# Optimization experiments

Hardware: AMD Instinct MI355X
Metric: run time of the kernel (lower is better)

Reference implementation:

```python
import jax, jax.numpy as jnp
import numpy as np

B, C, H, W = 4, 64, 64, 64
CQ = C // 8

def setup_inputs() -> dict:
    key = jax.random.key(0)
    ks = jax.random.split(key, 8)
    s = 1.0 / np.sqrt(C)
    return {
        "x": jax.random.normal(ks[0], (B, C, H, W), dtype=jnp.float32),
        "Wq": jax.random.normal(ks[1], (CQ, C), dtype=jnp.float32) * s,
        "bq": jax.random.normal(ks[2], (CQ,), dtype=jnp.float32) * 0.01,
        "Wk": jax.random.normal(ks[3], (CQ, C), dtype=jnp.float32) * s,
        "bk": jax.random.normal(ks[4], (CQ,), dtype=jnp.float32) * 0.01,
        "Wv": jax.random.normal(ks[5], (C, C), dtype=jnp.float32) * s,
        "bv": jax.random.normal(ks[6], (C,), dtype=jnp.float32) * 0.01,
        "gamma": jax.random.normal(ks[7], (1,), dtype=jnp.float32) * 0.1,
    }

def reference(x, Wq, bq, Wk, bk, Wv, bv, gamma):
    b, c, h, w = x.shape
    n = h * w
    xf = x.reshape(b, c, n)  # [B, C, N]
    # 1x1 convs are pointwise channel projections
    q = jnp.einsum('oc,bcn->bon', Wq, xf) + bq[None, :, None]  # [B, CQ, N]
    k = jnp.einsum('oc,bcn->bon', Wk, xf) + bk[None, :, None]  # [B, CQ, N]
    v = jnp.einsum('oc,bcn->bon', Wv, xf) + bv[None, :, None]  # [B, C, N]
    energy = jnp.einsum('bcn,bcm->bnm', q, k)                  # [B, N, N]
    attn = jax.nn.softmax(energy, axis=-1)
    out = jnp.einsum('bcm,bnm->bcn', v, attn)                  # [B, C, N]
    out = out.reshape(b, c, h, w)
    return gamma[0] * out + x
```

## Files before the change

### kernel.cpp

```cpp
#include <hip/hip_runtime.h>
#include <hip/hip_bf16.h>


typedef __attribute__((ext_vector_type(8))) short short8;
typedef __attribute__((ext_vector_type(4))) float f32x4;
typedef unsigned short ushort_t;

#define NSEQ 4096
#define LOG2E 1.4426950408889634f

__device__ __forceinline__ unsigned pk_bf16(float lo, float hi) {
  union { __hip_bfloat16 b; unsigned short u; } cl, ch;
  cl.b = __float2bfloat16(lo);
  ch.b = __float2bfloat16(hi);
  return (unsigned)cl.u | ((unsigned)ch.u << 16);
}

__global__ __launch_bounds__(256, 4) void proj_kernel(
    const float* __restrict__ x,
    const float* __restrict__ Wq, const float* __restrict__ bq,
    const float* __restrict__ Wk, const float* __restrict__ bk,
    const float* __restrict__ Wv, const float* __restrict__ bv,
    ushort_t* __restrict__ Qb, ushort_t* __restrict__ Kb,
    ushort_t* __restrict__ Vb)
{
  const int tid  = threadIdx.x;
  const int lane = tid & 63;
  const int w    = __builtin_amdgcn_readfirstlane(tid >> 6);
  const int blk  = blockIdx.x;
  const int quarter = blk & 3;
  const int g    = (blk >> 2) & 63;
  const int b    = blk >> 8;
  const int n    = g * 64 + lane;

  const float* xb = x + (size_t)(b * 64) * NSEQ + n;
  const int co0 = quarter * 16 + w * 4;
  const float* w0 = Wv + (co0 + 0) * 64;
  const float* w1 = Wv + (co0 + 1) * 64;
  const float* w2 = Wv + (co0 + 2) * 64;
  const float* w3 = Wv + (co0 + 3) * 64;
  const int p = quarter * 4 + w;
  const float* wr = (p < 8) ? (Wq + p * 64) : (Wk + (p - 8) * 64);
  float a0 = bv[co0 + 0], a1 = bv[co0 + 1], a2 = bv[co0 + 2], a3 = bv[co0 + 3];
  float aq = (p < 8) ? bq[p] : bk[p - 8];

#pragma unroll
  for (int kc = 0; kc < 64; kc += 8) {
    float xv[8];
#pragma unroll
    for (int i = 0; i < 8; ++i) xv[i] = xb[(size_t)(kc + i) * NSEQ];
#pragma unroll
    for (int i = 0; i < 8; ++i) {
      const float xk = xv[i];
      a0 += w0[kc + i] * xk;
      a1 += w1[kc + i] * xk;
      a2 += w2[kc + i] * xk;
      a3 += w3[kc + i] * xk;
      aq += wr[kc + i] * xk;
    }
  }

  union { __hip_bfloat16 h; ushort_t u; } cv;
  ushort_t* vt = Vb + ((size_t)(b * 128 + (n >> 5)) * 64 + co0) * 32 + (n & 31);
  cv.h = __float2bfloat16(a0); vt[0]  = cv.u;
  cv.h = __float2bfloat16(a1); vt[32] = cv.u;
  cv.h = __float2bfloat16(a2); vt[64] = cv.u;
  cv.h = __float2bfloat16(a3); vt[96] = cv.u;

  ushort_t* qk = ((p < 8) ? Qb : Kb) + ((size_t)(b * NSEQ + n)) * 8 + (p & 7);
  cv.h = __float2bfloat16(aq); *qk = cv.u;
}

__global__ __launch_bounds__(512, 4) void attn_kernel(
    const ushort_t* __restrict__ Qb, const ushort_t* __restrict__ Kb,
    const ushort_t* __restrict__ Vb, const float* __restrict__ x,
    const float* __restrict__ gamma, float* __restrict__ out)
{
  __shared__ unsigned P_lds[2][8][2][256];
  __shared__ float buf[4][64][36];

  const int tid  = threadIdx.x;
  const int wave = __builtin_amdgcn_readfirstlane(tid >> 6);
  const int lane = tid & 63;
  const int q16  = lane & 15;
  const int quad = lane >> 4;
  const int blk  = blockIdx.x;
  const int b    = blk >> 7;
  const int n0   = (blk & 127) << 5;
  const int mbase = wave << 9;

  const short8 z8 = {0, 0, 0, 0, 0, 0, 0, 0};
  short8 qfA = *(const short8*)(Qb + ((size_t)(b * NSEQ + n0 + q16)) * 8);
  short8 qfB = *(const short8*)(Qb + ((size_t)(b * NSEQ + n0 + 16 + q16)) * 8);
  if (quad != 0) { qfA = z8; qfB = z8; }

  const char* kbase = (const char*)(Kb + ((size_t)(b * NSEQ + mbase + q16)) * 8);
  const char* vbase = (const char*)(Vb + ((size_t)(b * 128 + (mbase >> 5)) * 64) * 32);
  const int voff = q16 * 64 + quad * 16;

  const int sw    = (q16 ^ (q16 >> 2)) & 3;
  const int row16 = q16 * 16;
  const int d0 = 2 * quad, d2 = 8 + 2 * quad;
  const int w00 = row16 + (((d0 >> 2) ^ sw) << 2) + (d0 & 3);
  const int w01 = row16 + ((((d0 + 1) >> 2) ^ sw) << 2) + ((d0 + 1) & 3);
  const int w10 = row16 + (((d2 >> 2) ^ sw) << 2) + (d2 & 3);
  const int w11 = row16 + ((((d2 + 1) >> 2) ^ sw) << 2) + ((d2 + 1) & 3);
  const int rdo = row16 + ((quad ^ sw) << 2);

  f32x4 aA0 = {0.f, 0.f, 0.f, 0.f};
  f32x4 aA1 = aA0, aA2 = aA0, aA3 = aA0;
  f32x4 aB0 = aA0, aB1 = aA0, aB2 = aA0, aB3 = aA0;
  float lA = 0.f, lB = 0.f;

  short8 kf0 = *(const short8*)(kbase);
  short8 kf1 = *(const short8*)(kbase + 256);
  short8 vf0 = *(const short8*)(vbase + voff);
  short8 vf1 = *(const short8*)(vbase + voff + 1024);
  short8 vf2 = *(const short8*)(vbase + voff + 2048);
  short8 vf3 = *(const short8*)(vbase + voff + 3072);

#pragma unroll 2
  for (int t = 0; t < 16; ++t) {
    const int tn = (t + 1 < 16) ? (t + 1) : 15;
    const size_t ko = (size_t)tn * 512;
    const size_t vo = (size_t)tn * 4096 + voff;
    short8 nk0 = *(const short8*)(kbase + ko);
    short8 nk1 = *(const short8*)(kbase + ko + 256);
    short8 nv0 = *(const short8*)(vbase + vo);
    short8 nv1 = *(const short8*)(vbase + vo + 1024);
    short8 nv2 = *(const short8*)(vbase + vo + 2048);
    short8 nv3 = *(const short8*)(vbase + vo + 3072);

    const f32x4 z = {0.f, 0.f, 0.f, 0.f};
    f32x4 s0 = __builtin_amdgcn_mfma_f32_16x16x32_bf16(kf0, qfA, z, 0, 0, 0);
    f32x4 s1 = __builtin_amdgcn_mfma_f32_16x16x32_bf16(kf1, qfA, z, 0, 0, 0);
    f32x4 s2 = __builtin_amdgcn_mfma_f32_16x16x32_bf16(kf0, qfB, z, 0, 0, 0);
    f32x4 s3 = __builtin_amdgcn_mfma_f32_16x16x32_bf16(kf1, qfB, z, 0, 0, 0);

    float pA0 = __builtin_amdgcn_exp2f(s0[0] * LOG2E);
    float pA1 = __builtin_amdgcn_exp2f(s0[1] * LOG2E);
    float pA2 = __builtin_amdgcn_exp2f(s0[2] * LOG2E);
    float pA3 = __builtin_amdgcn_exp2f(s0[3] * LOG2E);
    float pA4 = __builtin_amdgcn_exp2f(s1[0] * LOG2E);
    float pA5 = __builtin_amdgcn_exp2f(s1[1] * LOG2E);
    float pA6 = __builtin_amdgcn_exp2f(s1[2] * LOG2E);
    float pA7 = __builtin_amdgcn_exp2f(s1[3] * LOG2E);
    float pB0 = __builtin_amdgcn_exp2f(s2[0] * LOG2E);
    float pB1 = __builtin_amdgcn_exp2f(s2[1] * LOG2E);
    float pB2 = __builtin_amdgcn_exp2f(s2[2] * LOG2E);
    float pB3 = __builtin_amdgcn_exp2f(s2[3] * LOG2E);
    float pB4 = __builtin_amdgcn_exp2f(s3[0] * LOG2E);
    float pB5 = __builtin_amdgcn_exp2f(s3[1] * LOG2E);
    float pB6 = __builtin_amdgcn_exp2f(s3[2] * LOG2E);
    float pB7 = __builtin_amdgcn_exp2f(s3[3] * LOG2E);
    lA += ((pA0 + pA1) + (pA2 + pA3)) + ((pA4 + pA5) + (pA6 + pA7));
    lB += ((pB0 + pB1) + (pB2 + pB3)) + ((pB4 + pB5) + (pB6 + pB7));

    unsigned* pbA = &P_lds[t & 1][wave][0][0];
    unsigned* pbB = &P_lds[t & 1][wave][1][0];
    pbA[w00] = pk_bf16(pA0, pA1);
    pbA[w01] = pk_bf16(pA2, pA3);
    pbA[w10] = pk_bf16(pA4, pA5);
    pbA[w11] = pk_bf16(pA6, pA7);
    pbB[w00] = pk_bf16(pB0, pB1);
    pbB[w01] = pk_bf16(pB2, pB3);
    pbB[w10] = pk_bf16(pB4, pB5);
    pbB[w11] = pk_bf16(pB6, pB7);
    const short8 pfA = *(const short8*)(pbA + rdo);
    const short8 pfB = *(const short8*)(pbB + rdo);

    aA0 = __builtin_amdgcn_mfma_f32_16x16x32_bf16(pfA, vf0, aA0, 0, 0, 0);
    aA1 = __builtin_amdgcn_mfma_f32_16x16x32_bf16(pfA, vf1, aA1, 0, 0, 0);
    aA2 = __builtin_amdgcn_mfma_f32_16x16x32_bf16(pfA, vf2, aA2, 0, 0, 0);
    aA3 = __builtin_amdgcn_mfma_f32_16x16x32_bf16(pfA, vf3, aA3, 0, 0, 0);
    aB0 = __builtin_amdgcn_mfma_f32_16x16x32_bf16(pfB, vf0, aB0, 0, 0, 0);
    aB1 = __builtin_amdgcn_mfma_f32_16x16x32_bf16(pfB, vf1, aB1, 0, 0, 0);
    aB2 = __builtin_amdgcn_mfma_f32_16x16x32_bf16(pfB, vf2, aB2, 0, 0, 0);
    aB3 = __builtin_amdgcn_mfma_f32_16x16x32_bf16(pfB, vf3, aB3, 0, 0, 0);

    kf0 = nk0; kf1 = nk1;
    vf0 = nv0; vf1 = nv1; vf2 = nv2; vf3 = nv3;
  }

  lA += __shfl_xor(lA, 16); lA += __shfl_xor(lA, 32);
  lB += __shfl_xor(lB, 16); lB += __shfl_xor(lB, 32);

  f32x4 aAs[4] = {aA0, aA1, aA2, aA3};
  f32x4 aBs[4] = {aB0, aB1, aB2, aB3};

  if (wave >= 4) {
    float* d = &buf[wave - 4][lane][0];
#pragma unroll
    for (int j = 0; j < 4; ++j)
#pragma unroll
      for (int r = 0; r < 4; ++r) {
        d[j * 4 + r]      = aAs[j][r];
        d[16 + j * 4 + r] = aBs[j][r];
      }
    d[32] = lA; d[33] = lB;
  }
  __syncthreads();
  if (wave < 4) {
    float* d = &buf[wave][lane][0];
#pragma unroll
    for (int j = 0; j < 4; ++j)
#pragma unroll
      for (int r = 0; r < 4; ++r) {
        aAs[j][r] += d[j * 4 + r];
        aBs[j][r] += d[16 + j * 4 + r];
      }
    lA += d[32]; lB += d[33];
#pragma unroll
    for (int j = 0; j < 4; ++j)
#pragma unroll
      for (int r = 0; r < 4; ++r) {
        d[j * 4 + r]      = aAs[j][r];
        d[16 + j * 4 + r] = aBs[j][r];
      }
    d[32] = lA; d[33] = lB;
  }
  __syncthreads();

  const int qt = wave >> 2;
  const int cg = wave & 3;
  float fr[4] = {0.f, 0.f, 0.f, 0.f};
  float lt = 0.f;
#pragma unroll
  for (int w2 = 0; w2 < 4; ++w2) {
    lt += buf[w2][lane][32 + qt];
#pragma unroll
    for (int r = 0; r < 4; ++r) fr[r] += buf[w2][lane][qt * 16 + cg * 4 + r];
  }

  const float g = gamma[0];
  const int c = cg * 16 + q16;
#pragma unroll
  for (int r = 0; r < 4; ++r) {
    const int rr = quad * 4 + r;
    const float lr = __shfl(lt, rr);
    const size_t idx = ((size_t)(b * 64 + c)) * NSEQ + n0 + qt * 16 + rr;
    out[idx] = g * (fr[r] / lr) + x[idx];
  }
}

extern "C" void kernel_launch(void* const* d_in, const int* in_sizes, int n_in,
                              void* d_out, int out_size, void* d_ws, size_t ws_size,
                              hipStream_t stream) {
  (void)in_sizes; (void)n_in; (void)out_size; (void)ws_size;
  const float* x     = (const float*)d_in[0];
  const float* Wq    = (const float*)d_in[1];
  const float* bq    = (const float*)d_in[2];
  const float* Wk    = (const float*)d_in[3];
  const float* bk    = (const float*)d_in[4];
  const float* Wv    = (const float*)d_in[5];
  const float* bv    = (const float*)d_in[6];
  const float* gamma = (const float*)d_in[7];
  float* out = (float*)d_out;

  ushort_t* Qb = (ushort_t*)d_ws;
  ushort_t* Kb = (ushort_t*)((char*)d_ws + (256u << 10));
  ushort_t* Vb = (ushort_t*)((char*)d_ws + (512u << 10));

  hipLaunchKernelGGL(proj_kernel, dim3(1024), dim3(256), 0, stream,
                     x, Wq, bq, Wk, bk, Wv, bv, Qb, Kb, Vb);
  hipLaunchKernelGGL(attn_kernel, dim3(512), dim3(512), 0, stream,
                     Qb, Kb, Vb, x, gamma, out);
}
```

Before: 97.23 us.

## Keep softmax probabilities in registers via permuted K rows and transposed PV MFMA

The attention kernel now permutes the K row order and swaps the operands of the PV MFMA, so the exponentiated scores can be packed straight into MFMA operand registers. This drops the LDS round trip (and its swizzle) that previously re-laid out P each tile. The log2(e) factor is folded into Q inside the projection kernel, so the per-element multiply before exp2 goes away. The projection kernel is also restructured so each wave computes 16 V channels plus 4 Q/K channels per pixel, with packed 8-byte Q/K stores and a quarter of the blocks. The epilogue indexing changes to match the transposed accumulator layout. Risk: the fewer, larger projection blocks give less parallelism and more registers per thread.

```diff
diff --git a/kernel.cpp b/kernel.cpp
--- a/kernel.cpp
+++ b/kernel.cpp
@@ -16,7 +16,7 @@
   return (unsigned)cl.u | ((unsigned)ch.u << 16);
 }
 
-__global__ __launch_bounds__(256, 4) void proj_kernel(
+__global__ __launch_bounds__(256) void proj_kernel(
     const float* __restrict__ x,
     const float* __restrict__ Wq, const float* __restrict__ bq,
     const float* __restrict__ Wk, const float* __restrict__ bk,
@@ -28,21 +28,23 @@
   const int lane = tid & 63;
   const int w    = __builtin_amdgcn_readfirstlane(tid >> 6);
   const int blk  = blockIdx.x;
-  const int quarter = blk & 3;
-  const int g    = (blk >> 2) & 63;
-  const int b    = blk >> 8;
-  const int n    = g * 64 + lane;
+  const int b    = blk >> 6;
+  const int n    = (blk & 63) * 64 + lane;
 
   const float* xb = x + (size_t)(b * 64) * NSEQ + n;
-  const int co0 = quarter * 16 + w * 4;
-  const float* w0 = Wv + (co0 + 0) * 64;
-  const float* w1 = Wv + (co0 + 1) * 64;
-  const float* w2 = Wv + (co0 + 2) * 64;
-  const float* w3 = Wv + (co0 + 3) * 64;
-  const int p = quarter * 4 + w;
-  const float* wr = (p < 8) ? (Wq + p * 64) : (Wk + (p - 8) * 64);
-  float a0 = bv[co0 + 0], a1 = bv[co0 + 1], a2 = bv[co0 + 2], a3 = bv[co0 + 3];
-  float aq = (p < 8) ? bq[p] : bk[p - 8];
+
+  const int cv0 = w * 16;
+  float av[16];
+#pragma unroll
+  for (int j = 0; j < 16; ++j) av[j] = bv[cv0 + j];
+
+  const bool isq = (w < 2);
+  const int qkb  = (w & 1) * 4;
+  const float* Wr = isq ? Wq : Wk;
+  const float* br = isq ? bq : bk;
+  float aqk[4];
+#pragma unroll
+  for (int j = 0; j < 4; ++j) aqk[j] = br[qkb + j];
 
 #pragma unroll
   for (int kc = 0; kc < 64; kc += 8) {
@@ -52,23 +54,30 @@
 #pragma unroll
     for (int i = 0; i < 8; ++i) {
       const float xk = xv[i];
-      a0 += w0[kc + i] * xk;
-      a1 += w1[kc + i] * xk;
-      a2 += w2[kc + i] * xk;
-      a3 += w3[kc + i] * xk;
-      aq += wr[kc + i] * xk;
+#pragma unroll
+      for (int j = 0; j < 16; ++j) av[j] += Wv[(cv0 + j) * 64 + kc + i] * xk;
+#pragma unroll
+      for (int j = 0; j < 4; ++j) aqk[j] += Wr[(qkb + j) * 64 + kc + i] * xk;
     }
   }
 
   union { __hip_bfloat16 h; ushort_t u; } cv;
-  ushort_t* vt = Vb + ((size_t)(b * 128 + (n >> 5)) * 64 + co0) * 32 + (n & 31);
-  cv.h = __float2bfloat16(a0); vt[0]  = cv.u;
-  cv.h = __float2bfloat16(a1); vt[32] = cv.u;
-  cv.h = __float2bfloat16(a2); vt[64] = cv.u;
-  cv.h = __float2bfloat16(a3); vt[96] = cv.u;
-
-  ushort_t* qk = ((p < 8) ? Qb : Kb) + ((size_t)(b * NSEQ + n)) * 8 + (p & 7);
-  cv.h = __float2bfloat16(aq); *qk = cv.u;
+  ushort_t* vt = Vb + ((size_t)(b * 128 + (n >> 5)) * 64 + cv0) * 32 + (n & 31);
+#pragma unroll
+  for (int j = 0; j < 16; ++j) {
+    cv.h = __float2bfloat16(av[j]);
+    vt[j * 32] = cv.u;
+  }
+
+  if (isq) {
+#pragma unroll
+    for (int j = 0; j < 4; ++j) aqk[j] *= LOG2E;
+  }
+  union { unsigned u[2]; ulong1 l; } pkd;
+  pkd.u[0] = pk_bf16(aqk[0], aqk[1]);
+  pkd.u[1] = pk_bf16(aqk[2], aqk[3]);
+  ushort_t* qk = (isq ? Qb : Kb) + ((size_t)(b * NSEQ + n)) * 8 + qkb;
+  *(ulong1*)qk = pkd.l;
 }
 
 __global__ __launch_bounds__(512, 4) void attn_kernel(
@@ -76,7 +85,6 @@
     const ushort_t* __restrict__ Vb, const float* __restrict__ x,
     const float* __restrict__ gamma, float* __restrict__ out)
 {
-  __shared__ unsigned P_lds[2][8][2][256];
   __shared__ float buf[4][64][36];
 
   const int tid  = threadIdx.x;
@@ -94,18 +102,10 @@
   short8 qfB = *(const short8*)(Qb + ((size_t)(b * NSEQ + n0 + 16 + q16)) * 8);
   if (quad != 0) { qfA = z8; qfB = z8; }
 
-  const char* kbase = (const char*)(Kb + ((size_t)(b * NSEQ + mbase + q16)) * 8);
+  const int mperm = 8 * (q16 >> 2) + (q16 & 3);
+  const char* kbase = (const char*)(Kb + ((size_t)(b * NSEQ + mbase + mperm)) * 8);
   const char* vbase = (const char*)(Vb + ((size_t)(b * 128 + (mbase >> 5)) * 64) * 32);
   const int voff = q16 * 64 + quad * 16;
-
-  const int sw    = (q16 ^ (q16 >> 2)) & 3;
-  const int row16 = q16 * 16;
-  const int d0 = 2 * quad, d2 = 8 + 2 * quad;
-  const int w00 = row16 + (((d0 >> 2) ^ sw) << 2) + (d0 & 3);
-  const int w01 = row16 + ((((d0 + 1) >> 2) ^ sw) << 2) + ((d0 + 1) & 3);
-  const int w10 = row16 + (((d2 >> 2) ^ sw) << 2) + (d2 & 3);
-  const int w11 = row16 + ((((d2 + 1) >> 2) ^ sw) << 2) + ((d2 + 1) & 3);
-  const int rdo = row16 + ((quad ^ sw) << 2);
 
   f32x4 aA0 = {0.f, 0.f, 0.f, 0.f};
   f32x4 aA1 = aA0, aA2 = aA0, aA3 = aA0;
@@ -113,7 +113,7 @@
   float lA = 0.f, lB = 0.f;
 
   short8 kf0 = *(const short8*)(kbase);
-  short8 kf1 = *(const short8*)(kbase + 256);
+  short8 kf1 = *(const short8*)(kbase + 64);
   short8 vf0 = *(const short8*)(vbase + voff);
   short8 vf1 = *(const short8*)(vbase + voff + 1024);
   short8 vf2 = *(const short8*)(vbase + voff + 2048);
@@ -125,7 +125,7 @@
     const size_t ko = (size_t)tn * 512;
     const size_t vo = (size_t)tn * 4096 + voff;
     short8 nk0 = *(const short8*)(kbase + ko);
-    short8 nk1 = *(const short8*)(kbase + ko + 256);
+    short8 nk1 = *(const short8*)(kbase + ko + 64);
     short8 nv0 = *(const short8*)(vbase + vo);
     short8 nv1 = *(const short8*)(vbase + vo + 1024);
     short8 nv2 = *(const short8*)(vbase + vo + 2048);
@@ -137,46 +137,41 @@
     f32x4 s2 = __builtin_amdgcn_mfma_f32_16x16x32_bf16(kf0, qfB, z, 0, 0, 0);
     f32x4 s3 = __builtin_amdgcn_mfma_f32_16x16x32_bf16(kf1, qfB, z, 0, 0, 0);
 
-    float pA0 = __builtin_amdgcn_exp2f(s0[0] * LOG2E);
-    float pA1 = __builtin_amdgcn_exp2f(s0[1] * LOG2E);
-    float pA2 = __builtin_amdgcn_exp2f(s0[2] * LOG2E);
-    float pA3 = __builtin_amdgcn_exp2f(s0[3] * LOG2E);
-    float pA4 = __builtin_amdgcn_exp2f(s1[0] * LOG2E);
-    float pA5 = __builtin_amdgcn_exp2f(s1[1] * LOG2E);
-    float pA6 = __builtin_amdgcn_exp2f(s1[2] * LOG2E);
-    float pA7 = __builtin_amdgcn_exp2f(s1[3] * LOG2E);
-    float pB0 = __builtin_amdgcn_exp2f(s2[0] * LOG2E);
-    float pB1 = __builtin_amdgcn_exp2f(s2[1] * LOG2E);
-    float pB2 = __builtin_amdgcn_exp2f(s2[2] * LOG2E);
-    float pB3 = __builtin_amdgcn_exp2f(s2[3] * LOG2E);
-    float pB4 = __builtin_amdgcn_exp2f(s3[0] * LOG2E);
-    float pB5 = __builtin_amdgcn_exp2f(s3[1] * LOG2E);
-    float pB6 = __builtin_amdgcn_exp2f(s3[2] * LOG2E);
-    float pB7 = __builtin_amdgcn_exp2f(s3[3] * LOG2E);
+    float pA0 = __builtin_amdgcn_exp2f(s0[0]);
+    float pA1 = __builtin_amdgcn_exp2f(s0[1]);
+    float pA2 = __builtin_amdgcn_exp2f(s0[2]);
+    float pA3 = __builtin_amdgcn_exp2f(s0[3]);
+    float pA4 = __builtin_amdgcn_exp2f(s1[0]);
+    float pA5 = __builtin_amdgcn_exp2f(s1[1]);
+    float pA6 = __builtin_amdgcn_exp2f(s1[2]);
+    float pA7 = __builtin_amdgcn_exp2f(s1[3]);
+    float pB0 = __builtin_amdgcn_exp2f(s2[0]);
+    float pB1 = __builtin_amdgcn_exp2f(s2[1]);
+    float pB2 = __builtin_amdgcn_exp2f(s2[2]);
+    float pB3 = __builtin_amdgcn_exp2f(s2[3]);
+    float pB4 = __builtin_amdgcn_exp2f(s3[0]);
+    float pB5 = __builtin_amdgcn_exp2f(s3[1]);
+    float pB6 = __builtin_amdgcn_exp2f(s3[2]);
+    float pB7 = __builtin_amdgcn_exp2f(s3[3]);
     lA += ((pA0 + pA1) + (pA2 + pA3)) + ((pA4 + pA5) + (pA6 + pA7));
     lB += ((pB0 + pB1) + (pB2 + pB3)) + ((pB4 + pB5) + (pB6 + pB7));
 
-    unsigned* pbA = &P_lds[t & 1][wave][0][0];
-    unsigned* pbB = &P_lds[t & 1][wave][1][0];
-    pbA[w00] = pk_bf16(pA0, pA1);
-    pbA[w01] = pk_bf16(pA2, pA3);
-    pbA[w10] = pk_bf16(pA4, pA5);
-    pbA[w11] = pk_bf16(pA6, pA7);
-    pbB[w00] = pk_bf16(pB0, pB1);
-    pbB[w01] = pk_bf16(pB2, pB3);
-    pbB[w10] = pk_bf16(pB4, pB5);
-    pbB[w11] = pk_bf16(pB6, pB7);
-    const short8 pfA = *(const short8*)(pbA + rdo);
-    const short8 pfB = *(const short8*)(pbB + rdo);
-
-    aA0 = __builtin_amdgcn_mfma_f32_16x16x32_bf16(pfA, vf0, aA0, 0, 0, 0);
-    aA1 = __builtin_amdgcn_mfma_f32_16x16x32_bf16(pfA, vf1, aA1, 0, 0, 0);
-    aA2 = __builtin_amdgcn_mfma_f32_16x16x32_bf16(pfA, vf2, aA2, 0, 0, 0);
-    aA3 = __builtin_amdgcn_mfma_f32_16x16x32_bf16(pfA, vf3, aA3, 0, 0, 0);
-    aB0 = __builtin_amdgcn_mfma_f32_16x16x32_bf16(pfB, vf0, aB0, 0, 0, 0);
-    aB1 = __builtin_amdgcn_mfma_f32_16x16x32_bf16(pfB, vf1, aB1, 0, 0, 0);
-    aB2 = __builtin_amdgcn_mfma_f32_16x16x32_bf16(pfB, vf2, aB2, 0, 0, 0);
-    aB3 = __builtin_amdgcn_mfma_f32_16x16x32_bf16(pfB, vf3, aB3, 0, 0, 0);
+    union { unsigned u[4]; short8 s; } uA, uB;
+    uA.u[0] = pk_bf16(pA0, pA1); uA.u[1] = pk_bf16(pA2, pA3);
+    uA.u[2] = pk_bf16(pA4, pA5); uA.u[3] = pk_bf16(pA6, pA7);
+    uB.u[0] = pk_bf16(pB0, pB1); uB.u[1] = pk_bf16(pB2, pB3);
+    uB.u[2] = pk_bf16(pB4, pB5); uB.u[3] = pk_bf16(pB6, pB7);
+    const short8 pfA = uA.s;
+    const short8 pfB = uB.s;
+
+    aA0 = __builtin_amdgcn_mfma_f32_16x16x32_bf16(vf0, pfA, aA0, 0, 0, 0);
+    aA1 = __builtin_amdgcn_mfma_f32_16x16x32_bf16(vf1, pfA, aA1, 0, 0, 0);
+    aA2 = __builtin_amdgcn_mfma_f32_16x16x32_bf16(vf2, pfA, aA2, 0, 0, 0);
+    aA3 = __builtin_amdgcn_mfma_f32_16x16x32_bf16(vf3, pfA, aA3, 0, 0, 0);
+    aB0 = __builtin_amdgcn_mfma_f32_16x16x32_bf16(vf0, pfB, aB0, 0, 0, 0);
+    aB1 = __builtin_amdgcn_mfma_f32_16x16x32_bf16(vf1, pfB, aB1, 0, 0, 0);
+    aB2 = __builtin_amdgcn_mfma_f32_16x16x32_bf16(vf2, pfB, aB2, 0, 0, 0);
+    aB3 = __builtin_amdgcn_mfma_f32_16x16x32_bf16(vf3, pfB, aB3, 0, 0, 0);
 
     kf0 = nk0; kf1 = nk1;
     vf0 = nv0; vf1 = nv1; vf2 = nv2; vf3 = nv3;
@@ -233,13 +228,13 @@
   }
 
   const float g = gamma[0];
-  const int c = cg * 16 + q16;
+  const float ginv = g / lt;
+  const int nn = n0 + qt * 16 + q16;
 #pragma unroll
   for (int r = 0; r < 4; ++r) {
-    const int rr = quad * 4 + r;
-    const float lr = __shfl(lt, rr);
-    const size_t idx = ((size_t)(b * 64 + c)) * NSEQ + n0 + qt * 16 + rr;
-    out[idx] = g * (fr[r] / lr) + x[idx];
+    const int c = cg * 16 + quad * 4 + r;
+    const size_t idx = ((size_t)(b * 64 + c)) * NSEQ + nn;
+    out[idx] = fr[r] * ginv + x[idx];
   }
 }
 
@@ -261,7 +256,7 @@
   ushort_t* Kb = (ushort_t*)((char*)d_ws + (256u << 10));
   ushort_t* Vb = (ushort_t*)((char*)d_ws + (512u << 10));
 
-  hipLaunchKernelGGL(proj_kernel, dim3(1024), dim3(256), 0, stream,
+  hipLaunchKernelGGL(proj_kernel, dim3(256), dim3(256), 0, stream,
                      x, Wq, bq, Wk, bk, Wv, bv, Qb, Kb, Vb);
   hipLaunchKernelGGL(attn_kernel, dim3(512), dim3(512), 0, stream,
                      Qb, Kb, Vb, x, gamma, out);
```

After: 111.0 us. 1.14x slower.
